# Performance work log

Hardware: AMD Instinct MI355X
Metric: run time of the kernel (lower is better)

## Reference

```python
import jax, jax.numpy as jnp
import numpy as np

BLOCK = 128


def setup_inputs() -> dict:
    key = jax.random.key(0)
    k_x, k_w, k_s, k_b = jax.random.split(key, 4)
    B, S, IN, OUT = 2, 2048, 4096, 4096
    x = jax.random.normal(k_x, (B, S, IN), dtype=jnp.float32)
    # fp8-quantized weight values (simulate e4m3 rounding, keep fp32 storage)
    w = jax.random.normal(k_w, (OUT, IN), dtype=jnp.float32) * 0.02
    weight = w.astype(jnp.float8_e4m3fn).astype(jnp.float32)
    # per-128x128-block inverse scales
    weight_scale_inv = jax.random.uniform(
        k_s, (OUT // BLOCK, IN // BLOCK), dtype=jnp.float32, minval=0.5, maxval=1.5)
    bias = jax.random.normal(k_b, (OUT,), dtype=jnp.float32) * 0.01
    return {"x": x, "weight": weight, "weight_scale_inv": weight_scale_inv, "bias": bias}


def _dequant(weight, scale_inv):
    # weight: [O, I], scale_inv: [O/128, I/128] -> broadcast each scale over a 128x128 block
    O, I = weight.shape
    w = weight.reshape(O // BLOCK, BLOCK, I // BLOCK, BLOCK)
    w = w * scale_inv[:, None, :, None]
    return w.reshape(O, I)


def reference(x, weight, weight_scale_inv, bias):
    w_deq = _dequant(weight, weight_scale_inv)          # [O, I]
    out = jnp.einsum('bsi,oi->bso', x, w_deq)           # [B, S, O]
    return out + bias
```

## Files before the change

### kernel.cpp

```cpp
#include <hip/hip_runtime.h>
#include <hip/hip_bf16.h>
#include <stdint.h>

typedef __attribute__((ext_vector_type(4))) float f32x4;
typedef __attribute__((ext_vector_type(8))) short short8;

__device__ __forceinline__ ushort f2b(float f) {
    union { __hip_bfloat16 h; ushort u; } c;
    c.h = __float2bfloat16(f);
    return c.u;
}

__device__ __forceinline__ void gload_lds16(const void* g, void* lds) {
    __builtin_amdgcn_global_load_lds((const __attribute__((address_space(1))) void*)g,
                                     (__attribute__((address_space(3))) void*)lds,
                                     16, 0, 0);
}

#define BARRIER()  asm volatile("s_barrier" ::: "memory")
#define VMCNT2()   asm volatile("s_waitcnt vmcnt(2)" ::: "memory")

__global__ void conv_x_kernel(const float* __restrict__ x, ushort* __restrict__ xb, long n8) {
    long i = (long)blockIdx.x * blockDim.x + threadIdx.x;
    if (i >= n8) return;
    const float4* xv = (const float4*)x;
    float4 v0 = xv[i * 2], v1 = xv[i * 2 + 1];
    short8 r;
    r[0] = (short)f2b(v0.x); r[1] = (short)f2b(v0.y); r[2] = (short)f2b(v0.z); r[3] = (short)f2b(v0.w);
    r[4] = (short)f2b(v1.x); r[5] = (short)f2b(v1.y); r[6] = (short)f2b(v1.z); r[7] = (short)f2b(v1.w);
    *(short8*)&xb[i * 8] = r;
}

__global__ void conv_w_kernel(const float* __restrict__ w, const float* __restrict__ sinv,
                              ushort* __restrict__ wb, int K, int nbk) {
    const int o = blockIdx.y;
    const int c = (blockIdx.x * blockDim.x + threadIdx.x) * 8;
    if (c >= K) return;
    const float s = sinv[(o >> 7) * nbk + (c >> 7)];
    const float4* wv = (const float4*)(w + (size_t)o * K + c);
    float4 v0 = wv[0], v1 = wv[1];
    short8 r;
    r[0] = (short)f2b(v0.x * s); r[1] = (short)f2b(v0.y * s); r[2] = (short)f2b(v0.z * s); r[3] = (short)f2b(v0.w * s);
    r[4] = (short)f2b(v1.x * s); r[5] = (short)f2b(v1.y * s); r[6] = (short)f2b(v1.z * s); r[7] = (short)f2b(v1.w * s);
    *(short8*)&wb[(size_t)o * K + c] = r;
}

__global__ __launch_bounds__(512, 2)
void gemm256_kernel(const ushort* __restrict__ A, const ushort* __restrict__ Bm,
                    const float* __restrict__ bias, float* __restrict__ C,
                    int M, int N, int K) {
    __shared__ alignas(16) short sm[2][32768];

    const int tid  = threadIdx.x;
    const int lane = tid & 63;
    const int wid  = tid >> 6;
    const int wr   = wid >> 2;
    const int wc   = wid & 3;
    const int nbn  = N >> 8;

    const int nwg = gridDim.x;
    const int swz = (blockIdx.x & 7) * (nwg >> 3) + (blockIdx.x >> 3);
    const int bm  = swz / nbn;
    const int bn  = swz % nbn;

    const short* gA = (const short*)A + (size_t)bm * 256 * K;
    const short* gB = (const short*)Bm + (size_t)bn * 256 * K;

    const int srow = wid * 8 + (lane >> 3);
    const int scol = ((lane & 7) ^ (lane >> 3)) << 3;

    auto STAGE_A = [&](int U, int kt, int buf) {
        const short* src = gA + (size_t)(U * 64 + srow) * K + kt * 64 + scol;
        gload_lds16(src, &sm[buf][U * 4096 + wid * 512]);
    };
    auto STAGE_B = [&](int U, int kt, int buf) {
        const short* src = gB + (size_t)(U * 64 + srow) * K + kt * 64 + scol;
        gload_lds16(src, &sm[buf][16384 + U * 4096 + wid * 512]);
    };

    auto LD_A = [&](const short* Ab, int mh, int kk, short8 (&a)[4]) {
#pragma unroll
        for (int m = 0; m < 4; ++m) {
            int row = wr * 128 + mh * 64 + m * 16 + (lane & 15);
            a[m] = *(const short8*)&Ab[row * 64 + ((kk * 32 + (lane >> 4) * 8) ^ ((lane & 7) << 3))];
        }
    };
    auto LD_B = [&](const short* Bb, int kk, short8 (&b)[4]) {
#pragma unroll
        for (int n = 0; n < 4; ++n) {
            int row = wc * 64 + n * 16 + (lane & 15);
            b[n] = *(const short8*)&Bb[row * 64 + ((kk * 32 + (lane >> 4) * 8) ^ ((lane & 7) << 3))];
        }
    };

    f32x4 acc[8][4] = {};

    auto MFMA_H = [&](int off, short8 (&af)[4], short8 (&bf)[4], int m0, int m1) {
#pragma unroll
        for (int m = m0; m < m1; ++m)
#pragma unroll
            for (int n = 0; n < 4; ++n)
                acc[off + m][n] = __builtin_amdgcn_mfma_f32_16x16x32_bf16(af[m], bf[n], acc[off + m][n], 0, 0, 0);
    };

    const int nkt = K >> 6;

    auto KSTEP = [&](int t) {
        const int b  = t & 1;
        const int tb = b ^ 1;
        const short* Ab = &sm[b][0];
        const short* Bb = &sm[b][16384];
        const int tn  = (t + 1 < nkt) ? t + 1 : nkt - 1;
        const int tnn = (t + 2 < nkt) ? t + 2 : nkt - 1;

        short8 aA[4], aB[4], aC[4], aD[4], bA[4], bB[4];

        BARRIER();
        LD_A(Ab, 0, 0, aA);
        LD_B(Bb, 0, bA);
        __builtin_amdgcn_s_setprio(1);
        MFMA_H(0, aA, bA, 0, 2);
        LD_A(Ab, 1, 0, aB);
        MFMA_H(0, aA, bA, 2, 4);
        __builtin_amdgcn_s_setprio(0);
        STAGE_B(0, tn, tb); STAGE_B(1, tn, tb);

        BARRIER();
        __builtin_amdgcn_s_setprio(1);
        MFMA_H(4, aB, bA, 0, 2);
        LD_A(Ab, 0, 1, aC);
        LD_B(Bb, 1, bB);
        MFMA_H(4, aB, bA, 2, 4);
        __builtin_amdgcn_s_setprio(0);
        STAGE_A(1, tn, tb); STAGE_A(3, tn, tb);

        BARRIER();
        __builtin_amdgcn_s_setprio(1);
        MFMA_H(0, aC, bB, 0, 2);
        LD_A(Ab, 1, 1, aD);
        MFMA_H(0, aC, bB, 2, 4);
        __builtin_amdgcn_s_setprio(0);
        STAGE_B(2, tn, tb); STAGE_B(3, tn, tb);

        BARRIER();
        __builtin_amdgcn_s_setprio(1);
        MFMA_H(4, aD, bB, 0, 4);
        __builtin_amdgcn_s_setprio(0);
        STAGE_A(0, tnn, b); STAGE_A(2, tnn, b);
        VMCNT2();
    };

    {
        STAGE_B(0, 0, 0); STAGE_B(1, 0, 0);
        STAGE_A(1, 0, 0); STAGE_A(3, 0, 0);
        STAGE_B(2, 0, 0); STAGE_B(3, 0, 0);
        STAGE_A(0, 0, 0); STAGE_A(2, 0, 0);
        const int t1 = (nkt > 1) ? 1 : 0;
        STAGE_A(0, t1, 1); STAGE_A(2, t1, 1);
        VMCNT2();
    }

    for (int t = 0; t < nkt; t += 2) {
        KSTEP(t);
        KSTEP(t + 1);
    }

    const int r0 = bm * 256 + wr * 128 + (lane >> 4) * 4;
    const int c0 = bn * 256 + wc * 64 + (lane & 15);
#pragma unroll
    for (int n = 0; n < 4; ++n) {
        float bv = bias[c0 + n * 16];
#pragma unroll
        for (int m = 0; m < 8; ++m) {
#pragma unroll
            for (int r = 0; r < 4; ++r) {
                C[(size_t)(r0 + m * 16 + r) * N + (c0 + n * 16)] = acc[m][n][r] + bv;
            }
        }
    }
}

__global__ void fallback_gemm(const float* __restrict__ x, const float* __restrict__ w,
                              const float* __restrict__ sinv, const float* __restrict__ bias,
                              float* __restrict__ out, int M, int N, int K) {
    int n = blockIdx.x * 64 + (threadIdx.x & 63);
    int m = blockIdx.y * 4 + (threadIdx.x >> 6);
    if (m >= M || n >= N) return;
    const int nbk = K >> 7;
    float acc = 0.f;
    for (int k = 0; k < K; ++k)
        acc += x[(size_t)m * K + k] * w[(size_t)n * K + k] * sinv[(n >> 7) * nbk + (k >> 7)];
    out[(size_t)m * N + n] = acc + bias[n];
}

extern "C" void kernel_launch(void* const* d_in, const int* in_sizes, int n_in,
                              void* d_out, int out_size, void* d_ws, size_t ws_size,
                              hipStream_t stream) {
    const float* x    = (const float*)d_in[0];
    const float* w    = (const float*)d_in[1];
    const float* sinv = (const float*)d_in[2];
    const float* bias = (const float*)d_in[3];
    float* out        = (float*)d_out;

    const int O = in_sizes[3];
    const int K = in_sizes[1] / O;
    const int M = (int)((long)in_sizes[0] / K);
    const int N = O;

    const size_t need = ((size_t)M * K + (size_t)N * K) * sizeof(ushort);
    const int nwg = (M / 256) * (N / 256);
    const bool ok = ws_size >= need && (M % 256 == 0) && (N % 256 == 0) &&
                    (K % 128 == 0) && (nwg % 8 == 0) && ((long)M * K % 2048 == 0) &&
                    (K % 2048 == 0);
    if (ok) {
        ushort* xb = (ushort*)d_ws;
        ushort* wb = xb + (size_t)M * K;
        long n8 = (long)M * K / 8;
        conv_x_kernel<<<dim3((unsigned)(n8 / 256)), 256, 0, stream>>>(x, xb, n8);
        conv_w_kernel<<<dim3(K / 2048, N), 256, 0, stream>>>(w, sinv, wb, K, K >> 7);
        gemm256_kernel<<<dim3(nwg), 512, 0, stream>>>(xb, wb, bias, out, M, N, K);
    } else {
        dim3 g(N / 64, (M + 3) / 4);
        fallback_gemm<<<g, 256, 0, stream>>>(x, w, sinv, bias, out, M, N, K);
    }
}
```

Measured before the change: 279.3 us.

## Merge conversion kernels and simplify GEMM prefetch to single-step lookahead

The separate x and weight fp32-to-bf16 conversion kernels become one launch, using blockIdx.y to pick which tensor a block converts. This removes a kernel launch and lets both conversions share the GPU. The GEMM prefetch schedule is also restructured: the A-half that used to be fetched two k-steps ahead into the current buffer is now staged one step ahead into the other buffer, and each k-step ends with a full vmcnt(0) wait instead of vmcnt(2). This simplifies the pipeline but shortens the load lookahead and makes every step wait for all of its loads, which may expose more memory latency.

```diff
diff --git a/kernel.cpp b/kernel.cpp
--- a/kernel.cpp
+++ b/kernel.cpp
@@ -18,31 +18,34 @@
 }
 
 #define BARRIER()  asm volatile("s_barrier" ::: "memory")
-#define VMCNT2()   asm volatile("s_waitcnt vmcnt(2)" ::: "memory")
-
-__global__ void conv_x_kernel(const float* __restrict__ x, ushort* __restrict__ xb, long n8) {
+#define VMCNT0()   asm volatile("s_waitcnt vmcnt(0)" ::: "memory")
+
+__global__ void conv_both_kernel(const float* __restrict__ x, ushort* __restrict__ xb, long n8x,
+                                 const float* __restrict__ w, const float* __restrict__ sinv,
+                                 ushort* __restrict__ wb, int K, int nbk, long n8w) {
     long i = (long)blockIdx.x * blockDim.x + threadIdx.x;
-    if (i >= n8) return;
-    const float4* xv = (const float4*)x;
-    float4 v0 = xv[i * 2], v1 = xv[i * 2 + 1];
-    short8 r;
-    r[0] = (short)f2b(v0.x); r[1] = (short)f2b(v0.y); r[2] = (short)f2b(v0.z); r[3] = (short)f2b(v0.w);
-    r[4] = (short)f2b(v1.x); r[5] = (short)f2b(v1.y); r[6] = (short)f2b(v1.z); r[7] = (short)f2b(v1.w);
-    *(short8*)&xb[i * 8] = r;
-}
-
-__global__ void conv_w_kernel(const float* __restrict__ w, const float* __restrict__ sinv,
-                              ushort* __restrict__ wb, int K, int nbk) {
-    const int o = blockIdx.y;
-    const int c = (blockIdx.x * blockDim.x + threadIdx.x) * 8;
-    if (c >= K) return;
-    const float s = sinv[(o >> 7) * nbk + (c >> 7)];
-    const float4* wv = (const float4*)(w + (size_t)o * K + c);
-    float4 v0 = wv[0], v1 = wv[1];
-    short8 r;
-    r[0] = (short)f2b(v0.x * s); r[1] = (short)f2b(v0.y * s); r[2] = (short)f2b(v0.z * s); r[3] = (short)f2b(v0.w * s);
-    r[4] = (short)f2b(v1.x * s); r[5] = (short)f2b(v1.y * s); r[6] = (short)f2b(v1.z * s); r[7] = (short)f2b(v1.w * s);
-    *(short8*)&wb[(size_t)o * K + c] = r;
+    if (blockIdx.y == 0) {
+        if (i >= n8x) return;
+        const float4* xv = (const float4*)x;
+        float4 v0 = xv[i * 2], v1 = xv[i * 2 + 1];
+        short8 r;
+        r[0] = (short)f2b(v0.x); r[1] = (short)f2b(v0.y); r[2] = (short)f2b(v0.z); r[3] = (short)f2b(v0.w);
+        r[4] = (short)f2b(v1.x); r[5] = (short)f2b(v1.y); r[6] = (short)f2b(v1.z); r[7] = (short)f2b(v1.w);
+        *(short8*)&xb[i * 8] = r;
+    } else {
+        if (i >= n8w) return;
+        long e = i * 8;
+        int o, c;
+        if (K == 4096) { o = (int)(e >> 12); c = (int)(e & 4095); }
+        else { o = (int)(e / K); c = (int)(e - (long)o * K); }
+        const float s = sinv[(o >> 7) * nbk + (c >> 7)];
+        const float4* wv = (const float4*)(w + e);
+        float4 v0 = wv[0], v1 = wv[1];
+        short8 r;
+        r[0] = (short)f2b(v0.x * s); r[1] = (short)f2b(v0.y * s); r[2] = (short)f2b(v0.z * s); r[3] = (short)f2b(v0.w * s);
+        r[4] = (short)f2b(v1.x * s); r[5] = (short)f2b(v1.y * s); r[6] = (short)f2b(v1.z * s); r[7] = (short)f2b(v1.w * s);
+        *(short8*)&wb[e] = r;
+    }
 }
 
 __global__ __launch_bounds__(512, 2)
@@ -110,8 +113,7 @@
         const int tb = b ^ 1;
         const short* Ab = &sm[b][0];
         const short* Bb = &sm[b][16384];
-        const int tn  = (t + 1 < nkt) ? t + 1 : nkt - 1;
-        const int tnn = (t + 2 < nkt) ? t + 2 : nkt - 1;
+        const int tn = (t + 1 < nkt) ? t + 1 : nkt - 1;
 
         short8 aA[4], aB[4], aC[4], aD[4], bA[4], bB[4];
 
@@ -124,6 +126,7 @@
         MFMA_H(0, aA, bA, 2, 4);
         __builtin_amdgcn_s_setprio(0);
         STAGE_B(0, tn, tb); STAGE_B(1, tn, tb);
+        STAGE_A(0, tn, tb); STAGE_A(2, tn, tb);
 
         BARRIER();
         __builtin_amdgcn_s_setprio(1);
@@ -133,6 +136,7 @@
         MFMA_H(4, aB, bA, 2, 4);
         __builtin_amdgcn_s_setprio(0);
         STAGE_A(1, tn, tb); STAGE_A(3, tn, tb);
+        STAGE_B(2, tn, tb); STAGE_B(3, tn, tb);
 
         BARRIER();
         __builtin_amdgcn_s_setprio(1);
@@ -140,24 +144,20 @@
         LD_A(Ab, 1, 1, aD);
         MFMA_H(0, aC, bB, 2, 4);
         __builtin_amdgcn_s_setprio(0);
-        STAGE_B(2, tn, tb); STAGE_B(3, tn, tb);
 
         BARRIER();
         __builtin_amdgcn_s_setprio(1);
         MFMA_H(4, aD, bB, 0, 4);
         __builtin_amdgcn_s_setprio(0);
-        STAGE_A(0, tnn, b); STAGE_A(2, tnn, b);
-        VMCNT2();
+        VMCNT0();
     };
 
     {
         STAGE_B(0, 0, 0); STAGE_B(1, 0, 0);
+        STAGE_A(0, 0, 0); STAGE_A(2, 0, 0);
         STAGE_A(1, 0, 0); STAGE_A(3, 0, 0);
         STAGE_B(2, 0, 0); STAGE_B(3, 0, 0);
-        STAGE_A(0, 0, 0); STAGE_A(2, 0, 0);
-        const int t1 = (nkt > 1) ? 1 : 0;
-        STAGE_A(0, t1, 1); STAGE_A(2, t1, 1);
-        VMCNT2();
+        VMCNT0();
     }
 
     for (int t = 0; t < nkt; t += 2) {
@@ -215,9 +215,11 @@
     if (ok) {
         ushort* xb = (ushort*)d_ws;
         ushort* wb = xb + (size_t)M * K;
-        long n8 = (long)M * K / 8;
-        conv_x_kernel<<<dim3((unsigned)(n8 / 256)), 256, 0, stream>>>(x, xb, n8);
-        conv_w_kernel<<<dim3(K / 2048, N), 256, 0, stream>>>(w, sinv, wb, K, K >> 7);
+        long n8x = (long)M * K / 8;
+        long n8w = (long)N * K / 8;
+        long n8m = (n8x > n8w) ? n8x : n8w;
+        dim3 cg((unsigned)((n8m + 255) / 256), 2);
+        conv_both_kernel<<<cg, 256, 0, stream>>>(x, xb, n8x, w, sinv, wb, K, K >> 7, n8w);
         gemm256_kernel<<<dim3(nwg), 512, 0, stream>>>(xb, wb, bias, out, M, N, K);
     } else {
         dim3 g(N / 64, (M + 3) / 4);
```

Result: no change. 279.2 us (-0.0%).
